# Kernel tuning notes

Measured on AMD Instinct MI355X. Metric: run time of the kernel, lower is better.

Reference implementation:

```python
import jax, jax.numpy as jnp
import numpy as np

N, E, IN_C, HID, OUT_C, HEADS, NUM_CLASSES = 50000, 800000, 128, 64, 64, 4, 40
NEG_SLOPE = 0.2


def _gat_conv(x, src, dst, W, a_src, a_dst, bias, heads, concat):
    # x: [N, F_in]; W: [F_in, heads*C]; a_src/a_dst: [1, heads, C]; bias: [out]
    n = x.shape[0]
    h = (x @ W).reshape(n, heads, -1)                      # [N, H, C]
    alpha_s = (h * a_src).sum(-1)                          # [N, H]
    alpha_d = (h * a_dst).sum(-1)                          # [N, H]
    e = jax.nn.leaky_relu(alpha_s[src] + alpha_d[dst], NEG_SLOPE)  # [E, H]
    # scatter-softmax over incoming edges of each dst node
    emax = jax.ops.segment_max(e, dst, num_segments=n)
    emax = jnp.where(jnp.isfinite(emax), emax, 0.0)
    ee = jnp.exp(e - emax[dst])
    denom = jax.ops.segment_sum(ee, dst, num_segments=n) + 1e-16
    w = ee / denom[dst]                                    # [E, H]
    out = jax.ops.segment_sum(h[src] * w[:, :, None], dst, num_segments=n)  # [N, H, C]
    out = out.reshape(n, -1) if concat else out.mean(axis=1)
    return out + bias


def setup_inputs() -> dict:
    key = jax.random.key(0)
    ks = jax.random.split(key, 12)
    s1 = 1.0 / np.sqrt(IN_C)
    s2 = 1.0 / np.sqrt(HID * HEADS)
    s3 = 1.0 / np.sqrt(OUT_C)
    return {
        "x": jax.random.normal(ks[0], (N, IN_C), dtype=jnp.float32),
        "edge_index": jax.random.randint(ks[1], (2, E), 0, N, dtype=jnp.int64),
        "W1": jax.random.normal(ks[2], (IN_C, HEADS * HID), dtype=jnp.float32) * s1,
        "att_src1": jax.random.normal(ks[3], (1, HEADS, HID), dtype=jnp.float32) * s1,
        "att_dst1": jax.random.normal(ks[4], (1, HEADS, HID), dtype=jnp.float32) * s1,
        "b1": jnp.zeros((HEADS * HID,), dtype=jnp.float32),
        "W2": jax.random.normal(ks[5], (HEADS * HID, OUT_C), dtype=jnp.float32) * s2,
        "att_src2": jax.random.normal(ks[6], (1, 1, OUT_C), dtype=jnp.float32) * s2,
        "att_dst2": jax.random.normal(ks[7], (1, 1, OUT_C), dtype=jnp.float32) * s2,
        "b2": jnp.zeros((OUT_C,), dtype=jnp.float32),
        "fc_w": jax.random.normal(ks[8], (OUT_C, NUM_CLASSES), dtype=jnp.float32) * s3,
        "fc_b": jnp.zeros((NUM_CLASSES,), dtype=jnp.float32),
    }


def reference(x, edge_index, W1, att_src1, att_dst1, b1, W2, att_src2, att_dst2, b2, fc_w, fc_b):
    n = x.shape[0]
    loops = jnp.arange(n, dtype=edge_index.dtype)
    ei = jnp.concatenate([edge_index, jnp.stack([loops, loops])], axis=1)  # add self-loops (PyG default)
    src, dst = ei[0], ei[1]
    h = jax.nn.relu(_gat_conv(x, src, dst, W1, att_src1, att_dst1, b1, HEADS, True))
    h = jax.nn.relu(_gat_conv(h, src, dst, W2, att_src2, att_dst2, b2, 1, False))
    # dropout p=0.01 is identity in eval mode
    pooled = h.mean(axis=0, keepdims=True)                 # global mean pool -> [1, OUT_C]
    logits = pooled @ fc_w + fc_b
    return jax.nn.log_softmax(logits, axis=1)
```

## Files before the change

kernel.cpp:

```cpp
#include <hip/hip_runtime.h>
#include <hip/hip_bf16.h>
#include <math.h>

#define NEG_SLOPE 0.2f
#define CHUNK2 2048
#define PGROUPS 32

typedef __attribute__((ext_vector_type(8))) short bf16x8;
typedef __attribute__((ext_vector_type(4))) float f32x4;
typedef __attribute__((ext_vector_type(2))) float f32x2_t;

__device__ __forceinline__ float lrelu(float a) { return a >= 0.f ? a : NEG_SLOPE * a; }
__device__ __forceinline__ unsigned short f2bu(float v) {
  unsigned u = __float_as_uint(v);
  u += 0x7fffu + ((u >> 16) & 1u);
  return (unsigned short)(u >> 16);
}
__device__ __forceinline__ unsigned char f2fp8(float v) {
  return (unsigned char)(__builtin_amdgcn_cvt_pk_fp8_f32(v, v, 0, false) & 0xFF);
}
__device__ __forceinline__ void fp8x4_dec(unsigned v, float& a, float& b, float& c, float& d) {
  f32x2_t lo = __builtin_amdgcn_cvt_pk_f32_fp8(v, false);
  f32x2_t hi = __builtin_amdgcn_cvt_pk_f32_fp8(v, true);
  a = lo.x; b = lo.y; c = hi.x; d = hi.y;
}

__global__ __launch_bounds__(256) void prep_kernel(
    const float4* __restrict__ a0, ushort4* __restrict__ d0, int n0,
    const float4* __restrict__ a1, ushort4* __restrict__ d1, int n1,
    const float4* __restrict__ a2, ushort4* __restrict__ d2, int n2,
    const int* __restrict__ ei, int* __restrict__ bhist, int E0, int Etot, int NBUCK,
    int castBlocks, int histBlocks) {
  __shared__ int hsm[256];
  if (blockIdx.x < (unsigned)castBlocks) {
    int total = n0 + n1 + n2;
    for (int i = blockIdx.x * 256 + threadIdx.x; i < total; i += castBlocks * 256) {
      const float4* s;
      ushort4* d;
      int j = i;
      if (j < n0) { s = a0; d = d0; }
      else if (j < n0 + n1) { j -= n0; s = a1; d = d1; }
      else { j -= n0 + n1; s = a2; d = d2; }
      float4 v = s[j];
      d[j] = make_ushort4(f2bu(v.x), f2bu(v.y), f2bu(v.z), f2bu(v.w));
    }
  } else {
    int bid = blockIdx.x - castBlocks;
    int t = threadIdx.x;
    hsm[t] = 0;
    __syncthreads();
    for (int e = bid * 256 + t; e < Etot; e += histBlocks * 256) {
      int dst = (e < E0) ? ei[E0 + e] : (e - E0);
      atomicAdd(&hsm[dst >> 8], 1);
    }
    __syncthreads();
    if (t < NBUCK && hsm[t]) atomicAdd(&bhist[t], hsm[t]);
  }
}

__global__ __launch_bounds__(256) void bucket_scan_kernel(const int* __restrict__ bhist,
    int* __restrict__ bucketOff, int* __restrict__ cursor, int* __restrict__ rowptrN,
    int NBUCK, int Etot) {
  __shared__ int s[256];
  int t = threadIdx.x;
  int v = (t < NBUCK) ? bhist[t] : 0;
  s[t] = v;
  __syncthreads();
  for (int off = 1; off < 256; off <<= 1) {
    int u = (t >= off) ? s[t - off] : 0;
    __syncthreads();
    s[t] += u;
    __syncthreads();
  }
  int excl = s[t] - v;
  if (t < NBUCK) { bucketOff[t] = excl; cursor[t] = excl; }
  if (t == 0) { bucketOff[NBUCK] = Etot; *rowptrN = Etot; }
}

__device__ void gemm_tile(const unsigned short* __restrict__ A,
    const unsigned short* __restrict__ B, unsigned char* __restrict__ C8,
    const float* __restrict__ att_s, const float* __restrict__ att_d,
    float* __restrict__ as_, float* __restrict__ ad_,
    int M, int K, int Ncol, int H, int bx, int by, char* smem) {
  unsigned short (*Al)[40] = (unsigned short (*)[40])smem;
  unsigned short (*Bt)[40] = (unsigned short (*)[40])(smem + 5120);
  float* sal = (float*)(smem + 10240);
  float* sad = (float*)(smem + 10752);
  const int tid = threadIdx.x;
  const int row0 = by * 64, col0 = bx * 64;
  const int lane = tid & 63, wave = tid >> 6;
  const int wm = wave >> 1, wn = wave & 1;
  const int l15 = lane & 15, q = lane >> 4;

  f32x4 acc[2][2] = {};

  const int am = tid >> 2, ac = (tid & 3) * 8;
  const int bk = tid >> 3, bn = (tid & 7) * 8;

  for (int k0 = 0; k0 < K; k0 += 32) {
    ushort4 av0 = make_ushort4(0, 0, 0, 0), av1 = av0;
    if (row0 + am < M) {
      const ushort4* ap = (const ushort4*)(A + (size_t)(row0 + am) * K + k0 + ac);
      av0 = ap[0]; av1 = ap[1];
    }
    *(ushort4*)&Al[am][ac] = av0;
    *(ushort4*)&Al[am][ac + 4] = av1;
    {
      const ushort4* bp = (const ushort4*)(B + (size_t)(k0 + bk) * Ncol + col0 + bn);
      ushort4 b0 = bp[0], b1 = bp[1];
      Bt[bn + 0][bk] = b0.x; Bt[bn + 1][bk] = b0.y;
      Bt[bn + 2][bk] = b0.z; Bt[bn + 3][bk] = b0.w;
      Bt[bn + 4][bk] = b1.x; Bt[bn + 5][bk] = b1.y;
      Bt[bn + 6][bk] = b1.z; Bt[bn + 7][bk] = b1.w;
    }
    __syncthreads();
    bf16x8 af[2], bf[2];
#pragma unroll
    for (int mi = 0; mi < 2; mi++)
      af[mi] = *(const bf16x8*)&Al[wm * 32 + mi * 16 + l15][q * 8];
#pragma unroll
    for (int ni = 0; ni < 2; ni++)
      bf[ni] = *(const bf16x8*)&Bt[wn * 32 + ni * 16 + l15][q * 8];
#pragma unroll
    for (int mi = 0; mi < 2; mi++)
#pragma unroll
      for (int ni = 0; ni < 2; ni++)
        acc[mi][ni] = __builtin_amdgcn_mfma_f32_16x16x32_bf16(af[mi], bf[ni], acc[mi][ni], 0, 0, 0);
    __syncthreads();
  }
#pragma unroll
  for (int mi = 0; mi < 2; mi++) {
#pragma unroll
    for (int r = 0; r < 4; r++) {
      int grow = row0 + wm * 32 + mi * 16 + q * 4 + r;
      if (grow < M) {
#pragma unroll
        for (int ni = 0; ni < 2; ni++) {
          int gcol = col0 + wn * 32 + ni * 16 + l15;
          C8[(size_t)grow * Ncol + gcol] = f2fp8(acc[mi][ni][r]);
        }
      }
    }
  }
  float atts0 = att_s[col0 + wn * 32 + l15];
  float atts1 = att_s[col0 + wn * 32 + 16 + l15];
  float attd0 = att_d[col0 + wn * 32 + l15];
  float attd1 = att_d[col0 + wn * 32 + 16 + l15];
#pragma unroll
  for (int mi = 0; mi < 2; mi++) {
#pragma unroll
    for (int r = 0; r < 4; r++) {
      float vs = acc[mi][0][r] * atts0 + acc[mi][1][r] * atts1;
      float vd = acc[mi][0][r] * attd0 + acc[mi][1][r] * attd1;
#pragma unroll
      for (int off = 1; off < 16; off <<= 1) {
        vs += __shfl_xor(vs, off);
        vd += __shfl_xor(vd, off);
      }
      if (l15 == 0) {
        int rl = wm * 32 + mi * 16 + q * 4 + r;
        sal[wn * 64 + rl] = vs;
        sad[wn * 64 + rl] = vd;
      }
    }
  }
  __syncthreads();
  if (tid < 64) {
    int grow = row0 + tid;
    if (grow < M) {
      as_[(size_t)grow * H + bx] = sal[tid] + sal[64 + tid];
      ad_[(size_t)grow * H + bx] = sad[tid] + sad[64 + tid];
    }
  }
}

__global__ __launch_bounds__(256) void gemm_alpha_kernel(const unsigned short* __restrict__ A,
    const unsigned short* __restrict__ B, unsigned char* __restrict__ C8,
    const float* __restrict__ att_s, const float* __restrict__ att_d,
    float* __restrict__ as_, float* __restrict__ ad_, int M, int K, int Ncol, int H) {
  __shared__ __align__(16) char smem[11264];
  gemm_tile(A, B, C8, att_s, att_d, as_, ad_, M, K, Ncol, H, blockIdx.x, blockIdx.y, smem);
}

__global__ __launch_bounds__(256) void gemm1_scatter_kernel(
    const unsigned short* __restrict__ A, const unsigned short* __restrict__ B,
    unsigned char* __restrict__ C8, const float* __restrict__ att_s,
    const float* __restrict__ att_d, float* __restrict__ as_, float* __restrict__ ad_,
    int M, int K, int Ncol, int H, int GX,
    const int* __restrict__ ei, int* __restrict__ cursor, int* __restrict__ pairs,
    int E0, int Etot, int NBUCK, int NSC) {
  __shared__ __align__(16) char smem[18432];
  if (blockIdx.x < (unsigned)NSC) {
    int2* stage = (int2*)smem;
    int* h = (int*)(smem + 16384);
    int* base = (int*)(smem + 17408);
    int t = threadIdx.x;
    int e0 = blockIdx.x * CHUNK2;
    h[t] = 0;
    __syncthreads();
    int cnt = Etot - e0;
    if (cnt > CHUNK2) cnt = CHUNK2;
    for (int i = t; i < cnt; i += 256) {
      int e = e0 + i;
      int s, d;
      if (e < E0) { s = ei[e]; d = ei[E0 + e]; } else { s = d = e - E0; }
      stage[i] = make_int2((s << 8) | (d & 255), d >> 8);
      atomicAdd(&h[d >> 8], 1);
    }
    __syncthreads();
    if (t < NBUCK && h[t]) base[t] = atomicAdd(&cursor[t], h[t]);
    __syncthreads();
    for (int i = t; i < cnt; i += 256) {
      int2 p = stage[i];
      int pos = atomicAdd(&base[p.y], 1);
      pairs[pos] = p.x;
    }
  } else {
    int flat = blockIdx.x - NSC;
    gemm_tile(A, B, C8, att_s, att_d, as_, ad_, M, K, Ncol, H, flat % GX, flat / GX, smem);
  }
}

__global__ __launch_bounds__(256) void csr_build_kernel(const int* __restrict__ pairs,
    const int* __restrict__ bucketOff, int* __restrict__ rowptr, int* __restrict__ csr_src,
    int N) {
  int b = blockIdx.x, t = threadIdx.x;
  int base = bucketOff[b], cnt = bucketOff[b + 1] - base;
  int n0 = b << 8;
  __shared__ int h[256];
  __shared__ int s[256];
  __shared__ int ex[256];
  h[t] = 0;
  __syncthreads();
  for (int i = t; i < cnt; i += 256) atomicAdd(&h[pairs[base + i] & 255], 1);
  __syncthreads();
  int v = h[t];
  s[t] = v;
  __syncthreads();
  for (int off = 1; off < 256; off <<= 1) {
    int u = (t >= off) ? s[t - off] : 0;
    __syncthreads();
    s[t] += u;
    __syncthreads();
  }
  ex[t] = s[t] - v;
  if (n0 + t < N) rowptr[n0 + t] = base + ex[t];
  __syncthreads();
  for (int i = t; i < cnt; i += 256) {
    int p = pairs[base + i];
    int pos = atomicAdd(&ex[p & 255], 1);
    csr_src[base + pos] = ((unsigned)p) >> 8;
  }
}

__global__ __launch_bounds__(256) void aggr1_kernel(const int* __restrict__ rowptr,
    const int* __restrict__ csr_src, const float* __restrict__ as_,
    const float* __restrict__ ad_, const unsigned* __restrict__ h1f8,
    const float* __restrict__ b1, unsigned short* __restrict__ out1, int Nn) {
  int wv = threadIdx.x >> 6, lane = threadIdx.x & 63;
  int n = blockIdx.x * 4 + wv;
  if (n >= Nn) return;
  int row = rowptr[n], deg = rowptr[n + 1] - row;
  int hh = lane >> 4;
  float adv = ad_[n * 4 + hh];
  const unsigned* hb = h1f8 + lane;
  float a0 = 0.f, a1 = 0.f, a2 = 0.f, a3 = 0.f, wsum = 0.f;
  int s = 0;
  for (; s + 8 <= deg; s += 8) {
    int idx[8];
    float al[8];
    unsigned xv[8];
#pragma unroll
    for (int j = 0; j < 8; j++) idx[j] = csr_src[row + s + j];
#pragma unroll
    for (int j = 0; j < 8; j++) al[j] = as_[idx[j] * 4 + hh];
#pragma unroll
    for (int j = 0; j < 8; j++) xv[j] = hb[(size_t)idx[j] * 64];
#pragma unroll
    for (int j = 0; j < 8; j++) {
      float w = __expf(lrelu(al[j] + adv));
      wsum += w;
      float c0, c1, c2, c3;
      fp8x4_dec(xv[j], c0, c1, c2, c3);
      a0 = fmaf(w, c0, a0); a1 = fmaf(w, c1, a1);
      a2 = fmaf(w, c2, a2); a3 = fmaf(w, c3, a3);
    }
  }
  if (s + 4 <= deg) {
    int idx[4];
    float al[4];
    unsigned xv[4];
#pragma unroll
    for (int j = 0; j < 4; j++) idx[j] = csr_src[row + s + j];
#pragma unroll
    for (int j = 0; j < 4; j++) al[j] = as_[idx[j] * 4 + hh];
#pragma unroll
    for (int j = 0; j < 4; j++) xv[j] = hb[(size_t)idx[j] * 64];
#pragma unroll
    for (int j = 0; j < 4; j++) {
      float w = __expf(lrelu(al[j] + adv));
      wsum += w;
      float c0, c1, c2, c3;
      fp8x4_dec(xv[j], c0, c1, c2, c3);
      a0 = fmaf(w, c0, a0); a1 = fmaf(w, c1, a1);
      a2 = fmaf(w, c2, a2); a3 = fmaf(w, c3, a3);
    }
    s += 4;
  }
  for (; s < deg; s++) {
    int i0 = csr_src[row + s];
    float w = __expf(lrelu(as_[i0 * 4 + hh] + adv));
    wsum += w;
    float c0, c1, c2, c3;
    fp8x4_dec(hb[(size_t)i0 * 64], c0, c1, c2, c3);
    a0 = fmaf(w, c0, a0); a1 = fmaf(w, c1, a1);
    a2 = fmaf(w, c2, a2); a3 = fmaf(w, c3, a3);
  }
  float vinv = 1.f / wsum;
  int c0i = lane * 4;
  float4 bb = *(const float4*)(b1 + c0i);
  float rx = fmaf(a0, vinv, bb.x), ry = fmaf(a1, vinv, bb.y);
  float rz = fmaf(a2, vinv, bb.z), rw = fmaf(a3, vinv, bb.w);
  rx = rx > 0.f ? rx : 0.f; ry = ry > 0.f ? ry : 0.f;
  rz = rz > 0.f ? rz : 0.f; rw = rw > 0.f ? rw : 0.f;
  *(ushort4*)(out1 + (size_t)n * 256 + c0i) =
      make_ushort4(f2bu(rx), f2bu(ry), f2bu(rz), f2bu(rw));
}

__global__ __launch_bounds__(256) void aggr2_pool_kernel(const int* __restrict__ rowptr,
    const int* __restrict__ csr_src, const float* __restrict__ as_,
    const float* __restrict__ ad_, const unsigned* __restrict__ h2f8,
    const float* __restrict__ b2, float* __restrict__ pooled_grp, int Nn) {
  int lane = threadIdx.x & 63, wv = threadIdx.x >> 6;
  int q = lane >> 4, l15 = lane & 15;
  int c0 = l15 * 4;
  const unsigned* hb = h2f8 + l15;
  float p0 = 0.f, p1 = 0.f, p2 = 0.f, p3 = 0.f;
  int stream = (blockIdx.x * 4 + wv) * 4 + q;
  int nstreams = gridDim.x * 16;
  for (int n = stream; n < Nn; n += nstreams) {
    int row = rowptr[n], deg = rowptr[n + 1] - row;
    float adv = ad_[n];
    float a0 = 0.f, a1 = 0.f, a2 = 0.f, a3 = 0.f, wsum = 0.f;
    int s = 0;
    for (; s + 8 <= deg; s += 8) {
      int idx[8];
      float al[8];
      unsigned xv[8];
#pragma unroll
      for (int j = 0; j < 8; j++) idx[j] = csr_src[row + s + j];
#pragma unroll
      for (int j = 0; j < 8; j++) al[j] = as_[idx[j]];
#pragma unroll
      for (int j = 0; j < 8; j++) xv[j] = hb[(size_t)idx[j] * 16];
#pragma unroll
      for (int j = 0; j < 8; j++) {
        float w = __expf(lrelu(al[j] + adv));
        wsum += w;
        float c0f, c1f, c2f, c3f;
        fp8x4_dec(xv[j], c0f, c1f, c2f, c3f);
        a0 = fmaf(w, c0f, a0); a1 = fmaf(w, c1f, a1);
        a2 = fmaf(w, c2f, a2); a3 = fmaf(w, c3f, a3);
      }
    }
    if (s + 4 <= deg) {
      int idx[4];
      float al[4];
      unsigned xv[4];
#pragma unroll
      for (int j = 0; j < 4; j++) idx[j] = csr_src[row + s + j];
#pragma unroll
      for (int j = 0; j < 4; j++) al[j] = as_[idx[j]];
#pragma unroll
      for (int j = 0; j < 4; j++) xv[j] = hb[(size_t)idx[j] * 16];
#pragma unroll
      for (int j = 0; j < 4; j++) {
        float w = __expf(lrelu(al[j] + adv));
        wsum += w;
        float c0f, c1f, c2f, c3f;
        fp8x4_dec(xv[j], c0f, c1f, c2f, c3f);
        a0 = fmaf(w, c0f, a0); a1 = fmaf(w, c1f, a1);
        a2 = fmaf(w, c2f, a2); a3 = fmaf(w, c3f, a3);
      }
      s += 4;
    }
    for (; s < deg; s++) {
      int i0 = csr_src[row + s];
      float w = __expf(lrelu(as_[i0] + adv));
      wsum += w;
      float c0f, c1f, c2f, c3f;
      fp8x4_dec(hb[(size_t)i0 * 16], c0f, c1f, c2f, c3f);
      a0 = fmaf(w, c0f, a0); a1 = fmaf(w, c1f, a1);
      a2 = fmaf(w, c2f, a2); a3 = fmaf(w, c3f, a3);
    }
    float vinv = 1.f / wsum;
    float4 bb = *(const float4*)(b2 + c0);
    float r0 = fmaf(a0, vinv, bb.x), r1 = fmaf(a1, vinv, bb.y);
    float r2 = fmaf(a2, vinv, bb.z), r3 = fmaf(a3, vinv, bb.w);
    p0 += r0 > 0.f ? r0 : 0.f; p1 += r1 > 0.f ? r1 : 0.f;
    p2 += r2 > 0.f ? r2 : 0.f; p3 += r3 > 0.f ? r3 : 0.f;
  }
  __shared__ float4 sred[4][4][16];
  sred[wv][q][l15] = make_float4(p0, p1, p2, p3);
  __syncthreads();
  if (threadIdx.x < 64) {
    int slot = threadIdx.x >> 2, comp = threadIdx.x & 3;
    float acc = 0.f;
#pragma unroll
    for (int i = 0; i < 4; i++)
#pragma unroll
      for (int j = 0; j < 4; j++) {
        float4 v = sred[i][j][slot];
        acc += comp == 0 ? v.x : (comp == 1 ? v.y : (comp == 2 ? v.z : v.w));
      }
    atomicAdd(&pooled_grp[(blockIdx.x & (PGROUPS - 1)) * 64 + slot * 4 + comp], acc);
  }
}

__global__ __launch_bounds__(64) void pool_head_kernel(const float* __restrict__ pooled_grp,
    const float* __restrict__ fc_w, const float* __restrict__ fc_b,
    float* __restrict__ out, float invN) {
  int t = threadIdx.x;
  __shared__ float pl[64];
  __shared__ float lg[40];
  __shared__ float lse;
  float acc = 0.f;
#pragma unroll
  for (int g = 0; g < PGROUPS; g++) acc += pooled_grp[g * 64 + t];
  pl[t] = acc * invN;
  __syncthreads();
  if (t < 40) {
    float sm = fc_b[t];
    for (int c = 0; c < 64; c++) sm = fmaf(pl[c], fc_w[c * 40 + t], sm);
    lg[t] = sm;
  }
  __syncthreads();
  if (t == 0) {
    float m = -1e30f;
    for (int j = 0; j < 40; j++) m = fmaxf(m, lg[j]);
    float su = 0.f;
    for (int j = 0; j < 40; j++) su += expf(lg[j] - m);
    lse = m + logf(su);
  }
  __syncthreads();
  if (t < 40) out[t] = lg[t] - lse;
}

extern "C" void kernel_launch(void* const* d_in, const int* in_sizes, int n_in,
                              void* d_out, int out_size, void* d_ws, size_t ws_size,
                              hipStream_t stream) {
  const float* x        = (const float*)d_in[0];
  const int*   ei       = (const int*)d_in[1];
  const float* W1       = (const float*)d_in[2];
  const float* att_src1 = (const float*)d_in[3];
  const float* att_dst1 = (const float*)d_in[4];
  const float* b1       = (const float*)d_in[5];
  const float* W2       = (const float*)d_in[6];
  const float* att_src2 = (const float*)d_in[7];
  const float* att_dst2 = (const float*)d_in[8];
  const float* b2       = (const float*)d_in[9];
  const float* fc_w     = (const float*)d_in[10];
  const float* fc_b     = (const float*)d_in[11];
  float* out = (float*)d_out;

  const int N    = in_sizes[0] / 128;
  const int E0   = in_sizes[1] / 2;
  const int Etot = E0 + N;
  const int NBUCK = (N + 255) >> 8;
  const int NSC  = (Etot + CHUNK2 - 1) / CHUNK2;
  const int GBY  = (N + 63) / 64;
  const int AGG2_BLOCKS = 2048;

  char* wsb = (char*)d_ws;
  size_t o = 0;
  auto alloc = [&](size_t bytes) { char* p = wsb + o; o += (bytes + 15) & ~(size_t)15; return p; };
  unsigned short* xb   = (unsigned short*)alloc((size_t)N * 128 * 2);
  unsigned short* w1b  = (unsigned short*)alloc(128 * 256 * 2);
  unsigned short* w2b  = (unsigned short*)alloc(256 * 64 * 2);
  unsigned char*  h1f8 = (unsigned char*)alloc((size_t)N * 256);
  unsigned short* out1 = (unsigned short*)alloc((size_t)N * 256 * 2);
  float* as1  = (float*)alloc((size_t)N * 4 * 4);
  float* ad1  = (float*)alloc((size_t)N * 4 * 4);
  float* as2  = (float*)alloc((size_t)N * 4);
  float* ad2  = (float*)alloc((size_t)N * 4);
  int* rowptr = (int*)alloc((size_t)(N + 1) * 4);
  int* bhist  = (int*)alloc(256 * 4);
  int* bucketOff = (int*)alloc(257 * 4);
  int* cursor = (int*)alloc(256 * 4);
  int* pairs  = (int*)alloc((size_t)Etot * 4);
  int* csr_src = (int*)alloc((size_t)Etot * 4);
  float* pooled_grp = (float*)alloc((size_t)PGROUPS * 64 * 4);

  dim3 blk(256);

  hipMemsetAsync(bhist, 0, 256 * sizeof(int), stream);
  hipMemsetAsync(pooled_grp, 0, (size_t)PGROUPS * 64 * sizeof(float), stream);
  prep_kernel<<<512 + 256, blk, 0, stream>>>(
      (const float4*)x, (ushort4*)xb, N * 128 / 4,
      (const float4*)W1, (ushort4*)w1b, 128 * 256 / 4,
      (const float4*)W2, (ushort4*)w2b, 256 * 64 / 4,
      ei, bhist, E0, Etot, NBUCK, 512, 256);
  bucket_scan_kernel<<<1, blk, 0, stream>>>(bhist, bucketOff, cursor, rowptr + N, NBUCK, Etot);

  gemm1_scatter_kernel<<<NSC + 4 * GBY, blk, 0, stream>>>(
      xb, w1b, h1f8, att_src1, att_dst1, as1, ad1, N, 128, 256, 4, 4,
      ei, cursor, pairs, E0, Etot, NBUCK, NSC);
  csr_build_kernel<<<NBUCK, blk, 0, stream>>>(pairs, bucketOff, rowptr, csr_src, N);

  aggr1_kernel<<<(N + 3) / 4, blk, 0, stream>>>(rowptr, csr_src, as1, ad1,
                                                (const unsigned*)h1f8, b1, out1, N);

  gemm_alpha_kernel<<<dim3(1, GBY), blk, 0, stream>>>(out1, w2b, h1f8, att_src2, att_dst2,
                                                      as2, ad2, N, 256, 64, 1);
  aggr2_pool_kernel<<<AGG2_BLOCKS, blk, 0, stream>>>(rowptr, csr_src, as2, ad2,
                                                     (const unsigned*)h1f8, b2, pooled_grp, N);

  pool_head_kernel<<<1, 64, 0, stream>>>(pooled_grp, fc_w, fc_b, out, 1.0f / (float)N);
}
```

Baseline: 237.0 us.

## Assign one node per quarter-wave in layer-1 aggregation with 16-byte gathers

The layer-1 aggregation now handles four destination nodes per wavefront, one per 16-lane group. Each lane loads a uint4 (16 fp8 values) per neighbor instead of a single 32-bit word, and the degree loop is unrolled by 2 instead of 8. This is meant to cut per-node wave overhead and short-degree lane waste, and to widen each gather. In exchange each lane holds 16 accumulators, and fewer neighbor loads are in flight per lane, which could expose more memory latency.

Measured after the change: 237.4 us. No clear change (+0.2%).

```diff
diff --git a/kernel.cpp b/kernel.cpp
--- a/kernel.cpp
+++ b/kernel.cpp
@@ -255,76 +255,91 @@
 
 __global__ __launch_bounds__(256) void aggr1_kernel(const int* __restrict__ rowptr,
     const int* __restrict__ csr_src, const float* __restrict__ as_,
-    const float* __restrict__ ad_, const unsigned* __restrict__ h1f8,
+    const float* __restrict__ ad_, const uint4* __restrict__ h1f8,
     const float* __restrict__ b1, unsigned short* __restrict__ out1, int Nn) {
-  int wv = threadIdx.x >> 6, lane = threadIdx.x & 63;
-  int n = blockIdx.x * 4 + wv;
+  int lane = threadIdx.x & 63, wv = threadIdx.x >> 6;
+  int q = lane >> 4, l15 = lane & 15;
+  int n = (blockIdx.x * 4 + wv) * 4 + q;
   if (n >= Nn) return;
   int row = rowptr[n], deg = rowptr[n + 1] - row;
-  int hh = lane >> 4;
+  int hh = l15 >> 2;
   float adv = ad_[n * 4 + hh];
-  const unsigned* hb = h1f8 + lane;
-  float a0 = 0.f, a1 = 0.f, a2 = 0.f, a3 = 0.f, wsum = 0.f;
+  const uint4* hb = h1f8 + l15;
+  float acc[16] = {};
+  float wsum = 0.f;
   int s = 0;
-  for (; s + 8 <= deg; s += 8) {
-    int idx[8];
-    float al[8];
-    unsigned xv[8];
-#pragma unroll
-    for (int j = 0; j < 8; j++) idx[j] = csr_src[row + s + j];
-#pragma unroll
-    for (int j = 0; j < 8; j++) al[j] = as_[idx[j] * 4 + hh];
-#pragma unroll
-    for (int j = 0; j < 8; j++) xv[j] = hb[(size_t)idx[j] * 64];
-#pragma unroll
-    for (int j = 0; j < 8; j++) {
-      float w = __expf(lrelu(al[j] + adv));
-      wsum += w;
-      float c0, c1, c2, c3;
-      fp8x4_dec(xv[j], c0, c1, c2, c3);
-      a0 = fmaf(w, c0, a0); a1 = fmaf(w, c1, a1);
-      a2 = fmaf(w, c2, a2); a3 = fmaf(w, c3, a3);
-    }
-  }
-  if (s + 4 <= deg) {
-    int idx[4];
-    float al[4];
-    unsigned xv[4];
-#pragma unroll
-    for (int j = 0; j < 4; j++) idx[j] = csr_src[row + s + j];
-#pragma unroll
-    for (int j = 0; j < 4; j++) al[j] = as_[idx[j] * 4 + hh];
-#pragma unroll
-    for (int j = 0; j < 4; j++) xv[j] = hb[(size_t)idx[j] * 64];
-#pragma unroll
-    for (int j = 0; j < 4; j++) {
-      float w = __expf(lrelu(al[j] + adv));
-      wsum += w;
-      float c0, c1, c2, c3;
-      fp8x4_dec(xv[j], c0, c1, c2, c3);
-      a0 = fmaf(w, c0, a0); a1 = fmaf(w, c1, a1);
-      a2 = fmaf(w, c2, a2); a3 = fmaf(w, c3, a3);
-    }
-    s += 4;
-  }
-  for (; s < deg; s++) {
+  for (; s + 2 <= deg; s += 2) {
+    int i0 = csr_src[row + s], i1 = csr_src[row + s + 1];
+    float a0v = as_[i0 * 4 + hh], a1v = as_[i1 * 4 + hh];
+    uint4 x0 = hb[(size_t)i0 * 16];
+    uint4 x1 = hb[(size_t)i1 * 16];
+    float w0 = __expf(lrelu(a0v + adv));
+    float w1 = __expf(lrelu(a1v + adv));
+    wsum += w0 + w1;
+    float c0, c1, c2, c3;
+    fp8x4_dec(x0.x, c0, c1, c2, c3);
+    acc[0] = fmaf(w0, c0, acc[0]); acc[1] = fmaf(w0, c1, acc[1]);
+    acc[2] = fmaf(w0, c2, acc[2]); acc[3] = fmaf(w0, c3, acc[3]);
+    fp8x4_dec(x0.y, c0, c1, c2, c3);
+    acc[4] = fmaf(w0, c0, acc[4]); acc[5] = fmaf(w0, c1, acc[5]);
+    acc[6] = fmaf(w0, c2, acc[6]); acc[7] = fmaf(w0, c3, acc[7]);
+    fp8x4_dec(x0.z, c0, c1, c2, c3);
+    acc[8] = fmaf(w0, c0, acc[8]); acc[9] = fmaf(w0, c1, acc[9]);
+    acc[10] = fmaf(w0, c2, acc[10]); acc[11] = fmaf(w0, c3, acc[11]);
+    fp8x4_dec(x0.w, c0, c1, c2, c3);
+    acc[12] = fmaf(w0, c0, acc[12]); acc[13] = fmaf(w0, c1, acc[13]);
+    acc[14] = fmaf(w0, c2, acc[14]); acc[15] = fmaf(w0, c3, acc[15]);
+    fp8x4_dec(x1.x, c0, c1, c2, c3);
+    acc[0] = fmaf(w1, c0, acc[0]); acc[1] = fmaf(w1, c1, acc[1]);
+    acc[2] = fmaf(w1, c2, acc[2]); acc[3] = fmaf(w1, c3, acc[3]);
+    fp8x4_dec(x1.y, c0, c1, c2, c3);
+    acc[4] = fmaf(w1, c0, acc[4]); acc[5] = fmaf(w1, c1, acc[5]);
+    acc[6] = fmaf(w1, c2, acc[6]); acc[7] = fmaf(w1, c3, acc[7]);
+    fp8x4_dec(x1.z, c0, c1, c2, c3);
+    acc[8] = fmaf(w1, c0, acc[8]); acc[9] = fmaf(w1, c1, acc[9]);
+    acc[10] = fmaf(w1, c2, acc[10]); acc[11] = fmaf(w1, c3, acc[11]);
+    fp8x4_dec(x1.w, c0, c1, c2, c3);
+    acc[12] = fmaf(w1, c0, acc[12]); acc[13] = fmaf(w1, c1, acc[13]);
+    acc[14] = fmaf(w1, c2, acc[14]); acc[15] = fmaf(w1, c3, acc[15]);
+  }
+  if (s < deg) {
     int i0 = csr_src[row + s];
-    float w = __expf(lrelu(as_[i0 * 4 + hh] + adv));
-    wsum += w;
+    float w0 = __expf(lrelu(as_[i0 * 4 + hh] + adv));
+    wsum += w0;
+    uint4 x0 = hb[(size_t)i0 * 16];
     float c0, c1, c2, c3;
-    fp8x4_dec(hb[(size_t)i0 * 64], c0, c1, c2, c3);
-    a0 = fmaf(w, c0, a0); a1 = fmaf(w, c1, a1);
-    a2 = fmaf(w, c2, a2); a3 = fmaf(w, c3, a3);
+    fp8x4_dec(x0.x, c0, c1, c2, c3);
+    acc[0] = fmaf(w0, c0, acc[0]); acc[1] = fmaf(w0, c1, acc[1]);
+    acc[2] = fmaf(w0, c2, acc[2]); acc[3] = fmaf(w0, c3, acc[3]);
+    fp8x4_dec(x0.y, c0, c1, c2, c3);
+    acc[4] = fmaf(w0, c0, acc[4]); acc[5] = fmaf(w0, c1, acc[5]);
+    acc[6] = fmaf(w0, c2, acc[6]); acc[7] = fmaf(w0, c3, acc[7]);
+    fp8x4_dec(x0.z, c0, c1, c2, c3);
+    acc[8] = fmaf(w0, c0, acc[8]); acc[9] = fmaf(w0, c1, acc[9]);
+    acc[10] = fmaf(w0, c2, acc[10]); acc[11] = fmaf(w0, c3, acc[11]);
+    fp8x4_dec(x0.w, c0, c1, c2, c3);
+    acc[12] = fmaf(w0, c0, acc[12]); acc[13] = fmaf(w0, c1, acc[13]);
+    acc[14] = fmaf(w0, c2, acc[14]); acc[15] = fmaf(w0, c3, acc[15]);
   }
   float vinv = 1.f / wsum;
-  int c0i = lane * 4;
-  float4 bb = *(const float4*)(b1 + c0i);
-  float rx = fmaf(a0, vinv, bb.x), ry = fmaf(a1, vinv, bb.y);
-  float rz = fmaf(a2, vinv, bb.z), rw = fmaf(a3, vinv, bb.w);
-  rx = rx > 0.f ? rx : 0.f; ry = ry > 0.f ? ry : 0.f;
-  rz = rz > 0.f ? rz : 0.f; rw = rw > 0.f ? rw : 0.f;
-  *(ushort4*)(out1 + (size_t)n * 256 + c0i) =
-      make_ushort4(f2bu(rx), f2bu(ry), f2bu(rz), f2bu(rw));
+  int c0i = l15 * 16;
+  unsigned short ob[16];
+#pragma unroll
+  for (int k = 0; k < 4; k++) {
+    float4 bb = *(const float4*)(b1 + c0i + k * 4);
+    float r0 = fmaf(acc[k * 4 + 0], vinv, bb.x);
+    float r1 = fmaf(acc[k * 4 + 1], vinv, bb.y);
+    float r2 = fmaf(acc[k * 4 + 2], vinv, bb.z);
+    float r3 = fmaf(acc[k * 4 + 3], vinv, bb.w);
+    ob[k * 4 + 0] = f2bu(r0 > 0.f ? r0 : 0.f);
+    ob[k * 4 + 1] = f2bu(r1 > 0.f ? r1 : 0.f);
+    ob[k * 4 + 2] = f2bu(r2 > 0.f ? r2 : 0.f);
+    ob[k * 4 + 3] = f2bu(r3 > 0.f ? r3 : 0.f);
+  }
+  *(ushort4*)(out1 + (size_t)n * 256 + c0i) = *(ushort4*)&ob[0];
+  *(ushort4*)(out1 + (size_t)n * 256 + c0i + 4) = *(ushort4*)&ob[4];
+  *(ushort4*)(out1 + (size_t)n * 256 + c0i + 8) = *(ushort4*)&ob[8];
+  *(ushort4*)(out1 + (size_t)n * 256 + c0i + 12) = *(ushort4*)&ob[12];
 }
 
 __global__ __launch_bounds__(256) void aggr2_pool_kernel(const int* __restrict__ rowptr,
@@ -507,8 +522,8 @@
       ei, cursor, pairs, E0, Etot, NBUCK, NSC);
   csr_build_kernel<<<NBUCK, blk, 0, stream>>>(pairs, bucketOff, rowptr, csr_src, N);
 
-  aggr1_kernel<<<(N + 3) / 4, blk, 0, stream>>>(rowptr, csr_src, as1, ad1,
-                                                (const unsigned*)h1f8, b1, out1, N);
+  aggr1_kernel<<<(N + 15) / 16, blk, 0, stream>>>(rowptr, csr_src, as1, ad1,
+                                                  (const uint4*)h1f8, b1, out1, N);
 
   gemm_alpha_kernel<<<dim3(1, GBY), blk, 0, stream>>>(out1, w2b, h1f8, att_src2, att_dst2,
                                                       as2, ad2, N, 256, 64, 1);
```
